# Kernel tuning notes

Hardware: AMD Instinct MI355X
Metric: run time of the kernel (lower is better)

The kernel has to match this reference:

```python
import jax, jax.numpy as jnp
import numpy as np

H, P, T = 256, 16, 4      # hidden_size, maxout_pool_size, max_dec_steps
B, M = 32, 600            # batch, document length

def _lstm_cell(x, h, c, W_ih, W_hh, b_ih, b_hh):
    g = x @ W_ih.T + b_ih + h @ W_hh.T + b_hh
    i, f, gg, o = jnp.split(g, 4, axis=1)  # torch gate order i,f,g,o
    c = jax.nn.sigmoid(f) * c + jax.nn.sigmoid(i) * jnp.tanh(gg)
    h = jax.nn.sigmoid(o) * jnp.tanh(c)
    return h, c

def _maxout(h, U, u_cat, mask_mult, W_lin, W1, b1, W2, b2, W12, b12):
    b, m, _ = U.shape
    r = jnp.tanh(jnp.concatenate([h, u_cat], axis=1) @ W_lin.T)                  # [b,H]
    m1_in = jnp.concatenate([U, jnp.broadcast_to(r[:, None, :], (b, m, H))], 2)  # [b,m,3H]
    m1 = (m1_in @ W1.T + b1).reshape(b, m, H, P).max(-1)                         # [b,m,H]
    m2 = (m1 @ W2.T + b2).reshape(b, m, H, P).max(-1)                            # [b,m,H]
    alpha = (jnp.concatenate([m1, m2], axis=2) @ W12.T + b12).max(-1)            # [b,m]
    return jax.nn.log_softmax(alpha + mask_mult, axis=1)

def _forward(U, d_mask, span, W_ih, W_hh, b_ih, b_hh,
             Ws_lin, Ws_m1, bs_m1, Ws_m2, bs_m2, Ws_m12, bs_m12,
             We_lin, We_m1, be_m1, We_m2, be_m2, We_m12, be_m12):
    b, m, _ = U.shape
    idxb = jnp.arange(b)
    mask_mult = (1.0 - d_mask.astype(U.dtype)) * -1e30
    s_i = jnp.zeros(b, jnp.int32)
    e_i = (jnp.sum(d_mask, 1) - 1).astype(jnp.int32)
    s_tgt, e_tgt = span[:, 0], span[:, 1]
    h = jnp.zeros((b, H), U.dtype)
    c = jnp.zeros((b, H), U.dtype)
    mask_s = mask_e = None
    res_s, res_e, res_ms, res_me, losses = [], [], [], [], []
    u_s = U[idxb, s_i]
    for t in range(T):
        u_e = U[idxb, e_i]
        u_cat = jnp.concatenate([u_s, u_e], axis=1)
        h, c = _lstm_cell(u_cat, h, c, W_ih, W_hh, b_ih, b_hh)
        # start pointer
        lsm = _maxout(h, U, u_cat, mask_mult, Ws_lin, Ws_m1, bs_m1, Ws_m2, bs_m2, Ws_m12, bs_m12)
        idx = jnp.argmax(lsm, axis=1).astype(jnp.int32)
        if t == 0:
            mask_s = jnp.ones(b, bool)
        else:
            idx = idx * mask_s.astype(jnp.int32)
            prev = s_i * mask_s.astype(jnp.int32)
            mask_s = idx != prev
        loss_s = jnp.mean(-jnp.take_along_axis(lsm, s_tgt[:, None], 1)[:, 0]) * mask_s.astype(U.dtype)
        s_i = idx
        u_s = U[idxb, s_i]
        # end pointer
        u_cat2 = jnp.concatenate([u_s, u_e], axis=1)
        lsm_e = _maxout(h, U, u_cat2, mask_mult, We_lin, We_m1, be_m1, We_m2, be_m2, We_m12, be_m12)
        idx_e = jnp.argmax(lsm_e, axis=1).astype(jnp.int32)
        if t == 0:
            mask_e = jnp.ones(b, bool)
        else:
            idx_e = idx_e * mask_e.astype(jnp.int32)
            prev_e = e_i * mask_e.astype(jnp.int32)
            mask_e = idx_e != prev_e
        loss_e = jnp.mean(-jnp.take_along_axis(lsm_e, e_tgt[:, None], 1)[:, 0]) * mask_e.astype(U.dtype)
        e_i = idx_e
        losses.append(loss_s + loss_e)
        res_s.append(s_i); res_ms.append(mask_s)
        res_e.append(e_i); res_me.append(mask_e)
    pos_s = jnp.sum(jnp.stack(res_ms, 1).astype(jnp.int32), 1) - 1
    p1 = jnp.take_along_axis(jnp.stack(res_s, 1), pos_s[:, None], 1)[:, 0]
    pos_e = jnp.sum(jnp.stack(res_me, 1).astype(jnp.int32), 1) - 1
    p2 = jnp.take_along_axis(jnp.stack(res_e, 1), pos_e[:, None], 1)[:, 0]
    loss = jnp.mean(jnp.sum(jnp.stack(losses, 1), 1) / T)
    return loss, p1, p2

def setup_inputs():
    key = jax.random.key(0)
    ks = jax.random.split(key, 16)
    U = jax.random.normal(ks[0], (B, M, 2 * H), jnp.float32)
    lengths = jax.random.randint(ks[1], (B,), M // 2, M + 1)
    d_mask = (jnp.arange(M)[None, :] < lengths[:, None]).astype(jnp.int32)
    span = jax.random.randint(ks[2], (B, 2), 0, M // 2).astype(jnp.int32)
    def w(k, shape, fan_in):
        return (jax.random.normal(k, shape, jnp.float32) / np.float32(np.sqrt(fan_in)))
    b_ih = jnp.zeros(4 * H, jnp.float32).at[H:2 * H].set(1.0)  # forget-gate bias init
    params = {
        'W_ih': w(ks[3], (4 * H, 4 * H), 4 * H), 'W_hh': w(ks[4], (4 * H, H), H),
        'b_ih': b_ih, 'b_hh': jnp.zeros(4 * H, jnp.float32),
        'Ws_lin': w(ks[5], (H, 5 * H), 5 * H),
        'Ws_m1': w(ks[6], (H * P, 3 * H), 3 * H), 'bs_m1': jnp.zeros(H * P, jnp.float32),
        'Ws_m2': w(ks[7], (H * P, H), H), 'bs_m2': jnp.zeros(H * P, jnp.float32),
        'Ws_m12': w(ks[8], (P, 2 * H), 2 * H), 'bs_m12': jnp.zeros(P, jnp.float32),
        'We_lin': w(ks[9], (H, 5 * H), 5 * H),
        'We_m1': w(ks[10], (H * P, 3 * H), 3 * H), 'be_m1': jnp.zeros(H * P, jnp.float32),
        'We_m2': w(ks[11], (H * P, H), H), 'be_m2': jnp.zeros(H * P, jnp.float32),
        'We_m12': w(ks[12], (P, 2 * H), 2 * H), 'be_m12': jnp.zeros(P, jnp.float32),
    }
    return {'U': U, 'd_mask': d_mask, 'span': span, **params}

def reference(U, d_mask, span, W_ih, W_hh, b_ih, b_hh,
              Ws_lin, Ws_m1, bs_m1, Ws_m2, bs_m2, Ws_m12, bs_m12,
              We_lin, We_m1, be_m1, We_m2, be_m2, We_m12, be_m12):
    return _forward(U, d_mask, span, W_ih, W_hh, b_ih, b_hh,
                    Ws_lin, Ws_m1, bs_m1, Ws_m2, bs_m2, Ws_m12, bs_m12,
                    We_lin, We_m1, be_m1, We_m2, be_m2, We_m12, be_m12)
```

## Files before the change

### kernel.cpp

```cpp
#include <hip/hip_runtime.h>
#include <math.h>

namespace {

typedef unsigned short u16;
typedef __attribute__((ext_vector_type(4))) float f32x4;
typedef __attribute__((ext_vector_type(8))) _Float16 f16x8;
typedef __attribute__((ext_vector_type(4))) _Float16 f16x4;
typedef __attribute__((ext_vector_type(2))) _Float16 f16x2;

constexpr int B = 32;
constexpr int M = 600;
constexpr int H = 256;
constexpr int TSTEPS = 4;
constexpr int HP = 4096;
constexpr int BM = B * M;
constexpr int TWOH = 512;
constexpr int THREEH = 768;
constexpr int FOURH = 1024;
constexpr int FIVEH = 1280;
constexpr int NTILES = BM / 128;

__device__ __forceinline__ float sigf(float x) { return 1.0f / (1.0f + expf(-x)); }

__device__ __forceinline__ void gload16(const u16* g, u16* l) {
    __builtin_amdgcn_global_load_lds(
        (const __attribute__((address_space(1))) void*)g,
        (__attribute__((address_space(3))) void*)l, 16, 0, 0);
}

__global__ void k_init(const int* __restrict__ d_mask,
                       float* __restrict__ h, float* __restrict__ c,
                       float* __restrict__ loss_vec,
                       int* __restrict__ s_i, int* __restrict__ e_i,
                       int* __restrict__ p1r, int* __restrict__ p2r)
{
    int tid = threadIdx.x;
    for (int i = tid; i < B * H; i += 256) { h[i] = 0.f; c[i] = 0.f; }
    if (tid < B) {
        loss_vec[tid] = 0.f;
        s_i[tid] = 0;
        int s = 0;
        const int* row = d_mask + tid * M;
        for (int m = 0; m < M; ++m) s += row[m];
        e_i[tid] = s - 1;
        p1r[tid] = 0; p2r[tid] = 0;
    }
}

__global__ __launch_bounds__(128) void k_flags(const int* __restrict__ d_mask,
                                               int* __restrict__ flags)
{
    int bm = blockIdx.x * 128 + threadIdx.x;
    int cnt = __syncthreads_count(d_mask[bm]);
    if (threadIdx.x == 0) flags[blockIdx.x] = (cnt == 0) ? 1 : 0;
}

__global__ __launch_bounds__(256) void k_gather(
    const float* __restrict__ U, const int* __restrict__ s_i,
    const int* __restrict__ e_i, float* __restrict__ u_cat)
{
    int idx = blockIdx.x * 256 + threadIdx.x;
    int b = idx >> 9, k = idx & 511;
    u_cat[b * FOURH + k]       = U[((size_t)b * M + s_i[b]) * TWOH + k];
    u_cat[b * FOURH + 512 + k] = U[((size_t)b * M + e_i[b]) * TWOH + k];
}

__global__ __launch_bounds__(256) void k_lstm_gemm2(
    const float* __restrict__ U, const int* __restrict__ s_i,
    const int* __restrict__ e_i, const float* __restrict__ h,
    const float* __restrict__ W_ih, const float* __restrict__ W_hh,
    const float* __restrict__ b_ih, const float* __restrict__ b_hh,
    float* __restrict__ g)
{
    int idx = blockIdx.x * 256 + threadIdx.x;
    int b = idx >> 10, j = idx & 1023;
    const float* us = U + ((size_t)b * M + s_i[b]) * TWOH;
    const float* ue = U + ((size_t)b * M + e_i[b]) * TWOH;
    float acc = 0.f;
    const float4* x4 = (const float4*)us;
    const float4* wi4 = (const float4*)(W_ih + (size_t)j * FOURH);
    #pragma unroll 4
    for (int k = 0; k < TWOH / 4; ++k) {
        float4 a = x4[k], w = wi4[k];
        acc += a.x * w.x + a.y * w.y + a.z * w.z + a.w * w.w;
    }
    const float4* y4 = (const float4*)ue;
    const float4* wi4b = wi4 + TWOH / 4;
    #pragma unroll 4
    for (int k = 0; k < TWOH / 4; ++k) {
        float4 a = y4[k], w = wi4b[k];
        acc += a.x * w.x + a.y * w.y + a.z * w.z + a.w * w.w;
    }
    const float4* h4 = (const float4*)(h + b * H);
    const float4* wh4 = (const float4*)(W_hh + (size_t)j * H);
    #pragma unroll 4
    for (int k = 0; k < H / 4; ++k) {
        float4 a = h4[k], w = wh4[k];
        acc += a.x * w.x + a.y * w.y + a.z * w.z + a.w * w.w;
    }
    g[idx] = acc + b_ih[j] + b_hh[j];
}

__global__ __launch_bounds__(256) void k_lstm_gemm(
    const float* __restrict__ u_cat, const float* __restrict__ h,
    const float* __restrict__ W_ih, const float* __restrict__ W_hh,
    const float* __restrict__ b_ih, const float* __restrict__ b_hh,
    float* __restrict__ g)
{
    int idx = blockIdx.x * 256 + threadIdx.x;
    int b = idx >> 10, j = idx & 1023;
    float acc = 0.f;
    const float4* x4 = (const float4*)(u_cat + b * FOURH);
    const float4* wi4 = (const float4*)(W_ih + (size_t)j * FOURH);
    #pragma unroll 4
    for (int k = 0; k < FOURH / 4; ++k) {
        float4 a = x4[k], w = wi4[k];
        acc += a.x * w.x + a.y * w.y + a.z * w.z + a.w * w.w;
    }
    const float4* h4 = (const float4*)(h + b * H);
    const float4* wh4 = (const float4*)(W_hh + (size_t)j * H);
    #pragma unroll 4
    for (int k = 0; k < H / 4; ++k) {
        float4 a = h4[k], w = wh4[k];
        acc += a.x * w.x + a.y * w.y + a.z * w.z + a.w * w.w;
    }
    g[idx] = acc + b_ih[j] + b_hh[j];
}

__global__ __launch_bounds__(256) void k_lstm_gates(
    const float* __restrict__ g, float* __restrict__ h, float* __restrict__ c)
{
    int idx = blockIdx.x * 256 + threadIdx.x;
    int b = idx >> 8, i = idx & (H - 1);
    const float* gr = g + b * FOURH;
    float gi = gr[i], gf = gr[H + i], gg = gr[2 * H + i], go = gr[3 * H + i];
    float cn = sigf(gf) * c[idx] + sigf(gi) * tanhf(gg);
    c[idx] = cn;
    h[idx] = sigf(go) * tanhf(cn);
}

__global__ __launch_bounds__(256) void k_r2(
    const float* __restrict__ h, const float* __restrict__ U,
    const int* __restrict__ s_i, const int* __restrict__ e_i,
    const float* __restrict__ W_lin, float* __restrict__ r)
{
    int gid = blockIdx.x * 256 + threadIdx.x;
    int out = gid >> 2;
    int part = gid & 3;
    int b = out >> 8, i = out & (H - 1);
    const float4* w4 = (const float4*)(W_lin + (size_t)i * FIVEH);
    const float4* h4 = (const float4*)(h + b * H);
    const float4* us4 = (const float4*)(U + ((size_t)b * M + s_i[b]) * TWOH);
    const float4* ue4 = (const float4*)(U + ((size_t)b * M + e_i[b]) * TWOH);
    float acc = 0.f;
    int k0 = part * 80;
    #pragma unroll 4
    for (int kk = k0; kk < k0 + 80; ++kk) {
        float4 a;
        if (kk < 64) a = h4[kk];
        else if (kk < 192) a = us4[kk - 64];
        else a = ue4[kk - 192];
        float4 ww = w4[kk];
        acc += a.x * ww.x + a.y * ww.y + a.z * ww.z + a.w * ww.w;
    }
    acc += __shfl_xor(acc, 1);
    acc += __shfl_xor(acc, 2);
    if (part == 0) r[out] = tanhf(acc);
}

__global__ __launch_bounds__(256) void k_r(
    const float* __restrict__ h, const float* __restrict__ u_cat,
    const float* __restrict__ W_lin, float* __restrict__ r)
{
    int idx = blockIdx.x * 256 + threadIdx.x;
    int b = idx >> 8, i = idx & (H - 1);
    const float* w = W_lin + (size_t)i * FIVEH;
    float acc = 0.f;
    const float4* h4 = (const float4*)(h + b * H);
    const float4* w4 = (const float4*)w;
    #pragma unroll 4
    for (int k = 0; k < H / 4; ++k) {
        float4 a = h4[k], ww = w4[k];
        acc += a.x * ww.x + a.y * ww.y + a.z * ww.z + a.w * ww.w;
    }
    const float4* x4 = (const float4*)(u_cat + b * FOURH);
    const float4* w4b = (const float4*)(w + H);
    #pragma unroll 4
    for (int k = 0; k < FOURH / 4; ++k) {
        float4 a = x4[k], ww = w4b[k];
        acc += a.x * ww.x + a.y * ww.y + a.z * ww.z + a.w * ww.w;
    }
    r[idx] = tanhf(acc);
}

__global__ __launch_bounds__(256) void k_rW(
    const float* __restrict__ r, const float* __restrict__ W1,
    const float* __restrict__ b1, float* __restrict__ rW)
{
    int idx = blockIdx.x * 256 + threadIdx.x;
    int b = idx >> 12, j = idx & (HP - 1);
    const float4* r4 = (const float4*)(r + b * H);
    const float4* w4 = (const float4*)(W1 + (size_t)j * THREEH + TWOH);
    float acc = 0.f;
    #pragma unroll 4
    for (int k = 0; k < H / 4; ++k) {
        float4 a = r4[k], w = w4[k];
        acc += a.x * w.x + a.y * w.y + a.z * w.z + a.w * w.w;
    }
    rW[idx] = acc + b1[j];
}

__global__ __launch_bounds__(256) void k_rW2h(
    const float* __restrict__ r, const _Float16* __restrict__ Wt,
    const float* __restrict__ b1, float* __restrict__ rW)
{
    const int b = blockIdx.y;
    const int j = (blockIdx.x * 256 + threadIdx.x) * 2;
    __shared__ float sr[256];
    sr[threadIdx.x] = r[b * H + threadIdx.x];
    __syncthreads();
    float a0 = b1[j], a1 = b1[j + 1];
    #pragma unroll 4
    for (int k = 0; k < H; ++k) {
        f16x2 wv = *(const f16x2*)(Wt + (size_t)k * HP + j);
        float x = sr[k];
        a0 += x * (float)wv[0];
        a1 += x * (float)wv[1];
    }
    rW[(size_t)b * HP + j]     = a0;
    rW[(size_t)b * HP + j + 1] = a1;
}

__global__ __launch_bounds__(256) void k_transp2(
    const float* __restrict__ W, _Float16* __restrict__ Wt)
{
    __shared__ float s[32][33];
    int j0 = (blockIdx.x & 127) << 5;
    int k0 = (blockIdx.x >> 7) << 5;
    int tx = threadIdx.x & 31, ty = threadIdx.x >> 5;
    #pragma unroll
    for (int kk = 0; kk < 4; ++kk) {
        int jl = ty + kk * 8;
        s[jl][tx] = W[(size_t)(j0 + jl) * THREEH + TWOH + k0 + tx];
    }
    __syncthreads();
    #pragma unroll
    for (int kk = 0; kk < 4; ++kk) {
        int kl = ty + kk * 8;
        Wt[(size_t)(k0 + kl) * HP + j0 + tx] = (_Float16)s[tx][kl];
    }
}

__global__ __launch_bounds__(256) void k_cvtH(
    const float* __restrict__ src, int ld, int Kc, _Float16* __restrict__ dst)
{
    int i4 = blockIdx.x * 256 + threadIdx.x;
    int perrow = Kc >> 2;
    int row = i4 / perrow;
    int kc = (i4 - row * perrow) << 2;
    float4 v = *(const float4*)(src + (size_t)row * ld + kc);
    f16x4 o;
    o[0] = (_Float16)v.x; o[1] = (_Float16)v.y; o[2] = (_Float16)v.z; o[3] = (_Float16)v.w;
    *(f16x4*)(dst + (size_t)row * Kc + kc) = o;
}

template <int EPI>
__global__ __launch_bounds__(256, 4) void gemmJ(
    const _Float16* __restrict__ A, const _Float16* __restrict__ Bw,
    int K, const float* __restrict__ extra, const int* __restrict__ skip,
    float* __restrict__ Cf, _Float16* __restrict__ Ch)
{
    const int nwgx = gridDim.x;
    const int nwg  = nwgx * gridDim.y;
    int bid = blockIdx.y * nwgx + blockIdx.x;
    const int cpx = nwg >> 3;
    bid = (bid & 7) * cpx + (bid >> 3);
    const int bx = bid % nwgx, by = bid / nwgx;

    if (skip[by]) return;
    __shared__ __align__(16) u16 sA[2][128 * 32];
    __shared__ __align__(16) u16 sB[2][128 * 32];
    const int tid = threadIdx.x;
    const int w = tid >> 6, lane = tid & 63;
    const int row0 = by * 128, col0 = bx * 128;
    const int wm = w & 1, wn = w >> 1;

    const int r1g = tid >> 2,        k1 = (tid & 3) ^ ((r1g >> 1) & 3);
    const int r2g = (tid + 256) >> 2, k2 = ((tid + 256) & 3) ^ ((r2g >> 1) & 3);
    const size_t gA1 = (size_t)(row0 + r1g) * K + k1 * 8;
    const size_t gA2 = (size_t)(row0 + r2g) * K + k2 * 8;
    const size_t gB1 = (size_t)(col0 + r1g) * K + k1 * 8;
    const size_t gB2 = (size_t)(col0 + r2g) * K + k2 * 8;

    f32x4 acc[4][4] = {};

    gload16((const u16*)(A  + gA1), &sA[0][tid * 8]);
    gload16((const u16*)(A  + gA2), &sA[0][(tid + 256) * 8]);
    gload16((const u16*)(Bw + gB1), &sB[0][tid * 8]);
    gload16((const u16*)(Bw + gB2), &sB[0][(tid + 256) * 8]);

    const int iters = K >> 5;
    const int mrow = lane & 15;
    const int kg = lane >> 4;
    const int slot = kg ^ ((mrow >> 1) & 3);
    const int eoff = slot << 3;

    for (int it = 0; it < iters; ++it) {
        const int cur = it & 1;
        __syncthreads();
        if (it + 1 < iters) {
            const int k0n = (it + 1) << 5;
            gload16((const u16*)(A  + gA1 + k0n), &sA[1 - cur][tid * 8]);
            gload16((const u16*)(A  + gA2 + k0n), &sA[1 - cur][(tid + 256) * 8]);
            gload16((const u16*)(Bw + gB1 + k0n), &sB[1 - cur][tid * 8]);
            gload16((const u16*)(Bw + gB2 + k0n), &sB[1 - cur][(tid + 256) * 8]);
        }
        const u16* pa = &sA[cur][(wm * 64 + mrow) * 32 + eoff];
        const u16* pb = &sB[cur][(wn * 64 + mrow) * 32 + eoff];
        f16x8 fa[4], fb[4];
        #pragma unroll
        for (int f = 0; f < 4; ++f) {
            fa[f] = *(const f16x8*)(pa + f * 16 * 32);
            fb[f] = *(const f16x8*)(pb + f * 16 * 32);
        }
        #pragma unroll
        for (int i = 0; i < 4; ++i) {
            #pragma unroll
            for (int j = 0; j < 4; ++j) {
                acc[i][j] = __builtin_amdgcn_mfma_f32_16x16x32_f16(fa[i], fb[j], acc[i][j], 0, 0, 0);
            }
        }
    }

    const int cq = lane & 15, rq = lane >> 4;
    if (EPI == 4) {
        #pragma unroll
        for (int i = 0; i < 4; ++i) {
            #pragma unroll
            for (int j = 0; j < 4; ++j) {
                int col = col0 + wn * 64 + j * 16 + cq;
                #pragma unroll
                for (int rr = 0; rr < 4; ++rr) {
                    int row = row0 + wm * 64 + i * 16 + rq * 4 + rr;
                    Ch[(size_t)row * HP + col] = (_Float16)acc[i][j][rr];
                }
            }
        }
    } else if (EPI == 1) {
        #pragma unroll
        for (int j = 0; j < 4; ++j) {
            int col = col0 + wn * 64 + j * 16 + cq;
            int gcol = (col0 >> 4) + wn * 4 + j;
            float bv = extra[col];
            #pragma unroll
            for (int i = 0; i < 4; ++i) {
                #pragma unroll
                for (int rr = 0; rr < 4; ++rr) {
                    float v = acc[i][j][rr] + bv;
                    v = fmaxf(v, __shfl_xor(v, 1));
                    v = fmaxf(v, __shfl_xor(v, 2));
                    v = fmaxf(v, __shfl_xor(v, 4));
                    v = fmaxf(v, __shfl_xor(v, 8));
                    if (cq == 0) {
                        int row = row0 + wm * 64 + i * 16 + rq * 4 + rr;
                        Ch[(size_t)row * H + gcol] = (_Float16)v;
                    }
                }
            }
        }
    } else {
        const int rbase = row0 + wm * 64;
        const int b0 = rbase / M;
        const int bnd = (b0 + 1) * M;
        #pragma unroll
        for (int j = 0; j < 4; ++j) {
            int col = col0 + wn * 64 + j * 16 + cq;
            int gcol = (col0 >> 4) + wn * 4 + j;
            float e0 = extra[(size_t)b0 * HP + col];
            float e1 = extra[(size_t)(b0 + 1) * HP + col];
            #pragma unroll
            for (int i = 0; i < 4; ++i) {
                #pragma unroll
                for (int rr = 0; rr < 4; ++rr) {
                    int row = rbase + i * 16 + rq * 4 + rr;
                    float v = acc[i][j][rr] + ((row >= bnd) ? e1 : e0);
                    v = fmaxf(v, __shfl_xor(v, 1));
                    v = fmaxf(v, __shfl_xor(v, 2));
                    v = fmaxf(v, __shfl_xor(v, 4));
                    v = fmaxf(v, __shfl_xor(v, 8));
                    if (cq == 0)
                        Ch[(size_t)row * H + gcol] = (_Float16)v;
                }
            }
        }
    }
}

__global__ __launch_bounds__(256) void k_m1A16(
    const _Float16* __restrict__ A, const float* __restrict__ rW,
    _Float16* __restrict__ m1)
{
    int idx = blockIdx.x * 256 + threadIdx.x;
    int bm = idx >> 8;
    int h = idx & (H - 1);
    int b = bm / M;
    const f16x8* a8 = (const f16x8*)(A + (size_t)bm * HP + (h << 4));
    const float4* r4 = (const float4*)(rW + (size_t)b * HP + (h << 4));
    f16x8 a0 = a8[0], a1 = a8[1];
    float4 ra = r4[0], rb = r4[1], rc = r4[2], rd = r4[3];
    float mx;
    mx = fmaxf(fmaxf(fmaxf((float)a0[0] + ra.x, (float)a0[1] + ra.y),
                     fmaxf((float)a0[2] + ra.z, (float)a0[3] + ra.w)),
         fmaxf(fmaxf((float)a0[4] + rb.x, (float)a0[5] + rb.y),
               fmaxf((float)a0[6] + rb.z, (float)a0[7] + rb.w)));
    mx = fmaxf(mx,
         fmaxf(fmaxf(fmaxf((float)a1[0] + rc.x, (float)a1[1] + rc.y),
                     fmaxf((float)a1[2] + rc.z, (float)a1[3] + rc.w)),
               fmaxf(fmaxf((float)a1[4] + rd.x, (float)a1[5] + rd.y),
                     fmaxf((float)a1[6] + rd.z, (float)a1[7] + rd.w))));
    m1[idx] = (_Float16)mx;
}

template <int EPI>
__global__ __launch_bounds__(256) void gemm64(
    const float* __restrict__ Ag, int lda,
    const float* __restrict__ Bg, int ldb,
    const float* __restrict__ extra,
    float* __restrict__ C, int K, int ldc)
{
    __shared__ float As[16][68];
    __shared__ float Bs[16][68];
    const int tid = threadIdx.x;
    const int tx = tid & 15;
    const int ty = tid >> 4;
    const int row0 = blockIdx.y * 64;
    const int col0 = blockIdx.x * 64;
    const int lr = tid >> 2;
    const int lk = (tid & 3) << 2;
    const float* Aload = Ag + (size_t)(row0 + lr) * lda + lk;
    const float* Bload = Bg + (size_t)(col0 + lr) * ldb + lk;
    float acc[4][4] = {};
    for (int k0 = 0; k0 < K; k0 += 16) {
        float4 av = *(const float4*)(Aload + k0);
        float4 bv = *(const float4*)(Bload + k0);
        __syncthreads();
        As[lk + 0][lr] = av.x; As[lk + 1][lr] = av.y; As[lk + 2][lr] = av.z; As[lk + 3][lr] = av.w;
        Bs[lk + 0][lr] = bv.x; Bs[lk + 1][lr] = bv.y; Bs[lk + 2][lr] = bv.z; Bs[lk + 3][lr] = bv.w;
        __syncthreads();
        #pragma unroll
        for (int k = 0; k < 16; ++k) {
            float4 a4 = *(const float4*)(&As[k][ty << 2]);
            float4 b4 = *(const float4*)(&Bs[k][tx << 2]);
            acc[0][0] += a4.x * b4.x; acc[0][1] += a4.x * b4.y; acc[0][2] += a4.x * b4.z; acc[0][3] += a4.x * b4.w;
            acc[1][0] += a4.y * b4.x; acc[1][1] += a4.y * b4.y; acc[1][2] += a4.y * b4.z; acc[1][3] += a4.y * b4.w;
            acc[2][0] += a4.z * b4.x; acc[2][1] += a4.z * b4.y; acc[2][2] += a4.z * b4.z; acc[2][3] += a4.z * b4.w;
            acc[3][0] += a4.w * b4.x; acc[3][1] += a4.w * b4.y; acc[3][2] += a4.w * b4.z; acc[3][3] += a4.w * b4.w;
        }
    }
    if (EPI == 1) {
        const int cb = col0 + (tx << 2);
        float b0 = extra[cb], b1v = extra[cb + 1], b2v = extra[cb + 2], b3v = extra[cb + 3];
        #pragma unroll
        for (int i = 0; i < 4; ++i) {
            float mth = fmaxf(fmaxf(acc[i][0] + b0, acc[i][1] + b1v),
                              fmaxf(acc[i][2] + b2v, acc[i][3] + b3v));
            float r1 = fmaxf(mth, __shfl_xor(mth, 1));
            float r2 = fmaxf(r1, __shfl_xor(r1, 2));
            if ((tx & 3) == 0)
                C[(size_t)(row0 + (ty << 2) + i) * ldc + (col0 >> 4) + (tx >> 2)] = r2;
        }
    } else if (EPI == 2) {
        const int cb = col0 + (tx << 2);
        #pragma unroll
        for (int i = 0; i < 4; ++i) {
            int row = row0 + (ty << 2) + i;
            int b = row / M;
            const float* rw = extra + (size_t)b * HP + cb;
            float mth = fmaxf(fmaxf(acc[i][0] + rw[0], acc[i][1] + rw[1]),
                              fmaxf(acc[i][2] + rw[2], acc[i][3] + rw[3]));
            float r1 = fmaxf(mth, __shfl_xor(mth, 1));
            float r2 = fmaxf(r1, __shfl_xor(r1, 2));
            if ((tx & 3) == 0)
                C[(size_t)row * ldc + (col0 >> 4) + (tx >> 2)] = r2;
        }
    }
}

__global__ __launch_bounds__(256) void k_alpha(
    const float* __restrict__ m1, const float* __restrict__ m2,
    const float* __restrict__ W12, const float* __restrict__ b12,
    const int* __restrict__ d_mask, float* __restrict__ alpha)
{
    __shared__ float Ws[16 * 512];
    const int tid = threadIdx.x;
    for (int i = tid; i < 16 * 512; i += 256) Ws[i] = W12[i];
    __syncthreads();
    const int wave = tid >> 6, lane = tid & 63;
    const int bm = blockIdx.x * 4 + wave;
    const float* r1 = m1 + (size_t)bm * H;
    const float* r2 = m2 + (size_t)bm * H;
    float acc[16] = {};
    #pragma unroll
    for (int q = 0; q < 4; ++q) {
        int k = lane + (q << 6);
        float x = r1[k];
        #pragma unroll
        for (int p = 0; p < 16; ++p) acc[p] += x * Ws[p * 512 + k];
    }
    #pragma unroll
    for (int q = 0; q < 4; ++q) {
        int k = lane + (q << 6);
        float x = r2[k];
        #pragma unroll
        for (int p = 0; p < 16; ++p) acc[p] += x * Ws[p * 512 + 256 + k];
    }
    #pragma unroll
    for (int p = 0; p < 16; ++p) {
        float v = acc[p];
        v += __shfl_xor(v, 1);  v += __shfl_xor(v, 2);  v += __shfl_xor(v, 4);
        v += __shfl_xor(v, 8);  v += __shfl_xor(v, 16); v += __shfl_xor(v, 32);
        acc[p] = v;
    }
    if (lane == 0) {
        float mx = -INFINITY;
        #pragma unroll
        for (int p = 0; p < 16; ++p) mx = fmaxf(mx, acc[p] + b12[p]);
        alpha[bm] = d_mask[bm] ? mx : -1e30f;
    }
}

__global__ __launch_bounds__(256) void k_alphaM(
    const _Float16* __restrict__ m1, const _Float16* __restrict__ m2,
    const _Float16* __restrict__ W12h, const float* __restrict__ b12,
    const int* __restrict__ d_mask, float* __restrict__ alpha)
{
    const int wave = threadIdx.x >> 6, lane = threadIdx.x & 63;
    const int bm0 = blockIdx.x * 64 + wave * 16;
    const int rsel = lane & 15, kg = lane >> 4;
    f16x8 fb[16];
    #pragma unroll
    for (int kb = 0; kb < 16; ++kb)
        fb[kb] = *(const f16x8*)(W12h + (size_t)rsel * 512 + kb * 32 + kg * 8);
    f32x4 acc = {};
    const _Float16* r1 = m1 + (size_t)(bm0 + rsel) * H + kg * 8;
    const _Float16* r2 = m2 + (size_t)(bm0 + rsel) * H + kg * 8;
    #pragma unroll
    for (int kb = 0; kb < 8; ++kb) {
        f16x8 fa = *(const f16x8*)(r1 + kb * 32);
        acc = __builtin_amdgcn_mfma_f32_16x16x32_f16(fa, fb[kb], acc, 0, 0, 0);
    }
    #pragma unroll
    for (int kb = 0; kb < 8; ++kb) {
        f16x8 fa = *(const f16x8*)(r2 + kb * 32);
        acc = __builtin_amdgcn_mfma_f32_16x16x32_f16(fa, fb[8 + kb], acc, 0, 0, 0);
    }
    const int cq = lane & 15, rq = lane >> 4;
    float bv = b12[cq];
    #pragma unroll
    for (int reg = 0; reg < 4; ++reg) {
        float v = acc[reg] + bv;
        v = fmaxf(v, __shfl_xor(v, 1));
        v = fmaxf(v, __shfl_xor(v, 2));
        v = fmaxf(v, __shfl_xor(v, 4));
        v = fmaxf(v, __shfl_xor(v, 8));
        if (cq == 0) {
            int bm = bm0 + rq * 4 + reg;
            alpha[bm] = d_mask[bm] ? v : -1e30f;
        }
    }
}

__global__ __launch_bounds__(1024) void k_smu(
    const float* __restrict__ alpha, const int* __restrict__ span, int phase,
    int* __restrict__ pos, int* __restrict__ mask,
    int* __restrict__ prun, float* __restrict__ loss_vec, int t)
{
    __shared__ float s_loss[B];
    __shared__ int s_idx[B];
    const int wave = threadIdx.x >> 6, lane = threadIdx.x & 63;
    for (int b = wave; b < B; b += 16) {
        const float* row = alpha + b * M;
        float best = -INFINITY; int bidx = 0;
        for (int m = lane; m < M; m += 64) {
            float v = row[m];
            if (v > best) { best = v; bidx = m; }
        }
        #pragma unroll
        for (int off = 1; off < 64; off <<= 1) {
            float v2 = __shfl_xor(best, off);
            int i2 = __shfl_xor(bidx, off);
            if (v2 > best || (v2 == best && i2 < bidx)) { best = v2; bidx = i2; }
        }
        float ps = 0.f;
        for (int m = lane; m < M; m += 64) ps += expf(row[m] - best);
        #pragma unroll
        for (int off = 32; off > 0; off >>= 1) ps += __shfl_xor(ps, off);
        if (lane == 0) {
            float lse = best + logf(ps);
            int tgt = span[b * 2 + phase];
            s_loss[b] = -(row[tgt] - lse);
            s_idx[b] = bidx;
        }
    }
    __syncthreads();
    if (wave == 0) {
        int b = lane;
        int active = (b < B) ? 1 : 0;
        int ni = 0, nm = 0;
        if (active) {
            int id = s_idx[b];
            if (t == 0) { nm = 1; ni = id; }
            else {
                int om = mask[b];
                ni = id * om;
                int prev = pos[b] * om;
                nm = (ni != prev) ? 1 : 0;
            }
        }
        float v = active ? s_loss[b] : 0.f;
        #pragma unroll
        for (int off = 32; off > 0; off >>= 1) v += __shfl_xor(v, off);
        float S = v * (1.0f / (float)B);
        if (active) {
            pos[b] = ni;
            mask[b] = nm;
            if (nm) { prun[b] = ni; loss_vec[b] += S; }
        }
    }
}

__global__ __launch_bounds__(256) void k_softmax(
    const float* __restrict__ alpha, const int* __restrict__ span, int phase,
    float* __restrict__ loss_term, int* __restrict__ idx_out)
{
    __shared__ float sv[256];
    __shared__ int si[256];
    const int b = blockIdx.x, tid = threadIdx.x;
    const float* row = alpha + b * M;
    float best = -INFINITY; int bidx = 0;
    for (int m = tid; m < M; m += 256) {
        float v = row[m];
        if (v > best) { best = v; bidx = m; }
    }
    sv[tid] = best; si[tid] = bidx;
    __syncthreads();
    for (int s = 128; s > 0; s >>= 1) {
        if (tid < s) {
            float v2 = sv[tid + s]; int i2 = si[tid + s];
            if (v2 > sv[tid] || (v2 == sv[tid] && i2 < si[tid])) { sv[tid] = v2; si[tid] = i2; }
        }
        __syncthreads();
    }
    float bmax = sv[0]; int amax = si[0];
    __syncthreads();
    float ps = 0.f;
    for (int m = tid; m < M; m += 256) ps += expf(row[m] - bmax);
    sv[tid] = ps;
    __syncthreads();
    for (int s = 128; s > 0; s >>= 1) {
        if (tid < s) sv[tid] += sv[tid + s];
        __syncthreads();
    }
    if (tid == 0) {
        float lse = bmax + logf(sv[0]);
        int tgt = span[b * 2 + phase];
        loss_term[b] = -(row[tgt] - lse);
        idx_out[b] = amax;
    }
}

__global__ void k_update(const int* __restrict__ idx_in, const float* __restrict__ loss_term,
                         int* __restrict__ pos, int* __restrict__ mask,
                         int* __restrict__ prun, float* __restrict__ loss_vec, int t)
{
    int b = threadIdx.x;
    int active = (b < B) ? 1 : 0;
    int ni = 0, nm = 0;
    if (active) {
        int id = idx_in[b];
        if (t == 0) { nm = 1; ni = id; }
        else {
            int om = mask[b];
            ni = id * om;
            int prev = pos[b] * om;
            nm = (ni != prev) ? 1 : 0;
        }
    }
    float v = active ? loss_term[b] : 0.f;
    #pragma unroll
    for (int off = 32; off > 0; off >>= 1) v += __shfl_xor(v, off);
    float S = v * (1.0f / (float)B);
    if (active) {
        pos[b] = ni;
        mask[b] = nm;
        if (nm) { prun[b] = ni; loss_vec[b] += S; }
    }
}

__global__ void k_finalize(const float* __restrict__ loss_vec, const int* __restrict__ p1r,
                           const int* __restrict__ p2r, float* __restrict__ out)
{
    int b = threadIdx.x;
    float v = (b < B) ? loss_vec[b] : 0.f;
    #pragma unroll
    for (int off = 32; off > 0; off >>= 1) v += __shfl_xor(v, off);
    if (b == 0) out[0] = v / (float)(B * TSTEPS);
    if (b < B) {
        out[1 + b] = (float)p1r[b];
        out[1 + B + b] = (float)p2r[b];
    }
}

}

extern "C" void kernel_launch(void* const* d_in, const int* in_sizes, int n_in,
                              void* d_out, int out_size, void* d_ws, size_t ws_size,
                              hipStream_t stream)
{
    const float* U      = (const float*)d_in[0];
    const int*   d_mask = (const int*)d_in[1];
    const int*   span   = (const int*)d_in[2];
    const float* W_ih   = (const float*)d_in[3];
    const float* W_hh   = (const float*)d_in[4];
    const float* b_ih   = (const float*)d_in[5];
    const float* b_hh   = (const float*)d_in[6];
    const float* Ws_lin = (const float*)d_in[7];
    const float* Ws_m1  = (const float*)d_in[8];
    const float* bs_m1  = (const float*)d_in[9];
    const float* Ws_m2  = (const float*)d_in[10];
    const float* bs_m2  = (const float*)d_in[11];
    const float* Ws_m12 = (const float*)d_in[12];
    const float* bs_m12 = (const float*)d_in[13];
    const float* We_lin = (const float*)d_in[14];
    const float* We_m1  = (const float*)d_in[15];
    const float* be_m1  = (const float*)d_in[16];
    const float* We_m2  = (const float*)d_in[17];
    const float* be_m2  = (const float*)d_in[18];
    const float* We_m12 = (const float*)d_in[19];
    const float* be_m12 = (const float*)d_in[20];

    float* ws = (float*)d_ws;
    size_t o = 0;
    float* m2b   = ws + o; o += (size_t)BM * H;
    float* alphab= ws + o; o += BM;
    float* u_cat = ws + o; o += B * FOURH;
    float* gbuf  = ws + o; o += B * FOURH;
    float* hbuf  = ws + o; o += B * H;
    float* cbuf  = ws + o; o += B * H;
    float* rbuf  = ws + o; o += B * H;
    float* rWb   = ws + o; o += B * HP;
    float* loss_term = ws + o; o += B;
    float* loss_vec  = ws + o; o += B;
    int* ib = (int*)(ws + o); o += 8 * B + 160;
    int* idxb   = ib + 0 * B;
    int* s_i    = ib + 1 * B;
    int* e_i    = ib + 2 * B;
    int* mask_s = ib + 3 * B;
    int* mask_e = ib + 4 * B;
    int* p1r    = ib + 5 * B;
    int* p2r    = ib + 6 * B;
    int* flags  = ib + 8 * B;
    size_t o_common = (o + 3) & ~(size_t)3;

    float* m1b = ws + o_common;

    _Float16* hs = (_Float16*)(ws + o_common);
    size_t q = 0;
    _Float16* Uh    = hs + q; q += (size_t)BM * TWOH;
    _Float16* W1s   = hs + q; q += (size_t)HP * TWOH;
    _Float16* W1e   = hs + q; q += (size_t)HP * TWOH;
    _Float16* W2s   = hs + q; q += (size_t)HP * H;
    _Float16* W2e   = hs + q; q += (size_t)HP * H;
    _Float16* m1b16 = hs + q; q += (size_t)BM * H;
    _Float16* Wth_s = hs + q; q += (size_t)H * HP;
    _Float16* Wth_e = hs + q; q += (size_t)H * HP;
    _Float16* W12sh = hs + q; q += 16 * 512;
    _Float16* W12eh = hs + q; q += 16 * 512;
    q = (q + 7) & ~(size_t)7;
    const size_t need2 = o_common * sizeof(float) + q * sizeof(_Float16);
    _Float16* A_s16 = hs + q;
    _Float16* A_e16 = A_s16 + (size_t)BM * HP;
    const size_t need15s = need2 + (size_t)BM * HP * sizeof(_Float16);
    const size_t need16  = need15s + (size_t)BM * HP * sizeof(_Float16);

    _Float16* m2h = (_Float16*)m2b;

    const int tier = (ws_size >= need16) ? 16
                   : (ws_size >= need15s) ? 15
                   : (ws_size >= need2) ? 2 : 3;

    k_init<<<1, 256, 0, stream>>>(d_mask, hbuf, cbuf, loss_vec, s_i, e_i, p1r, p2r);

    if (tier != 3) {
        k_flags<<<NTILES, 128, 0, stream>>>(d_mask, flags);
        k_cvtH<<<BM * TWOH / 4 / 256, 256, 0, stream>>>(U, TWOH, TWOH, Uh);
        k_cvtH<<<HP * TWOH / 4 / 256, 256, 0, stream>>>(Ws_m1, THREEH, TWOH, W1s);
        k_cvtH<<<HP * TWOH / 4 / 256, 256, 0, stream>>>(We_m1, THREEH, TWOH, W1e);
        k_cvtH<<<HP * H / 4 / 256, 256, 0, stream>>>(Ws_m2, H, H, W2s);
        k_cvtH<<<HP * H / 4 / 256, 256, 0, stream>>>(We_m2, H, H, W2e);
        k_cvtH<<<16 * 512 / 4 / 256, 256, 0, stream>>>(Ws_m12, 512, 512, W12sh);
        k_cvtH<<<16 * 512 / 4 / 256, 256, 0, stream>>>(We_m12, 512, 512, W12eh);
        k_transp2<<<1024, 256, 0, stream>>>(Ws_m1, Wth_s);
        k_transp2<<<1024, 256, 0, stream>>>(We_m1, Wth_e);

        dim3 gJ(HP / 128, NTILES);
        if (tier >= 15) {
            gemmJ<4><<<gJ, 256, 0, stream>>>(Uh, W1s, TWOH, nullptr, flags, nullptr, A_s16);
        }
        if (tier == 16) {
            gemmJ<4><<<gJ, 256, 0, stream>>>(Uh, W1e, TWOH, nullptr, flags, nullptr, A_e16);
        }

        for (int t = 0; t < TSTEPS; ++t) {
            k_lstm_gemm2<<<128, 256, 0, stream>>>(U, s_i, e_i, hbuf, W_ih, W_hh, b_ih, b_hh, gbuf);
            k_lstm_gates<<<32, 256, 0, stream>>>(gbuf, hbuf, cbuf);

            k_r2<<<128, 256, 0, stream>>>(hbuf, U, s_i, e_i, Ws_lin, rbuf);
            k_rW2h<<<dim3(HP / 512, B), 256, 0, stream>>>(rbuf, Wth_s, bs_m1, rWb);
            if (tier >= 15)
                k_m1A16<<<BM * H / 256, 256, 0, stream>>>(A_s16, rWb, m1b16);
            else
                gemmJ<3><<<gJ, 256, 0, stream>>>(Uh, W1s, TWOH, rWb, flags, nullptr, m1b16);
            gemmJ<1><<<gJ, 256, 0, stream>>>(m1b16, W2s, H, bs_m2, flags, nullptr, m2h);
            k_alphaM<<<BM / 64, 256, 0, stream>>>(m1b16, m2h, W12sh, bs_m12, d_mask, alphab);
            k_smu<<<1, 1024, 0, stream>>>(alphab, span, 0, s_i, mask_s, p1r, loss_vec, t);

            k_r2<<<128, 256, 0, stream>>>(hbuf, U, s_i, e_i, We_lin, rbuf);
            k_rW2h<<<dim3(HP / 512, B), 256, 0, stream>>>(rbuf, Wth_e, be_m1, rWb);
            if (tier == 16)
                k_m1A16<<<BM * H / 256, 256, 0, stream>>>(A_e16, rWb, m1b16);
            else
                gemmJ<3><<<gJ, 256, 0, stream>>>(Uh, W1e, TWOH, rWb, flags, nullptr, m1b16);
            gemmJ<1><<<gJ, 256, 0, stream>>>(m1b16, W2e, H, be_m2, flags, nullptr, m2h);
            k_alphaM<<<BM / 64, 256, 0, stream>>>(m1b16, m2h, W12eh, be_m12, d_mask, alphab);
            k_smu<<<1, 1024, 0, stream>>>(alphab, span, 1, e_i, mask_e, p2r, loss_vec, t);
        }
    } else {
        dim3 gemm_grid(HP / 64, BM / 64);
        for (int t = 0; t < TSTEPS; ++t) {
            k_gather<<<64, 256, 0, stream>>>(U, s_i, e_i, u_cat);
            k_lstm_gemm<<<128, 256, 0, stream>>>(u_cat, hbuf, W_ih, W_hh, b_ih, b_hh, gbuf);
            k_lstm_gates<<<32, 256, 0, stream>>>(gbuf, hbuf, cbuf);

            k_r<<<32, 256, 0, stream>>>(hbuf, u_cat, Ws_lin, rbuf);
            k_rW<<<512, 256, 0, stream>>>(rbuf, Ws_m1, bs_m1, rWb);
            gemm64<2><<<gemm_grid, 256, 0, stream>>>(U, TWOH, Ws_m1, THREEH, rWb, m1b, TWOH, H);
            gemm64<1><<<gemm_grid, 256, 0, stream>>>(m1b, H, Ws_m2, H, bs_m2, m2b, H, H);
            k_alpha<<<BM / 4, 256, 0, stream>>>(m1b, m2b, Ws_m12, bs_m12, d_mask, alphab);
            k_softmax<<<B, 256, 0, stream>>>(alphab, span, 0, loss_term, idxb);
            k_update<<<1, 64, 0, stream>>>(idxb, loss_term, s_i, mask_s, p1r, loss_vec, t);

            k_gather<<<64, 256, 0, stream>>>(U, s_i, e_i, u_cat);

            k_r<<<32, 256, 0, stream>>>(hbuf, u_cat, We_lin, rbuf);
            k_rW<<<512, 256, 0, stream>>>(rbuf, We_m1, be_m1, rWb);
            gemm64<2><<<gemm_grid, 256, 0, stream>>>(U, TWOH, We_m1, THREEH, rWb, m1b, TWOH, H);
            gemm64<1><<<gemm_grid, 256, 0, stream>>>(m1b, H, We_m2, H, be_m2, m2b, H, H);
            k_alpha<<<BM / 4, 256, 0, stream>>>(m1b, m2b, We_m12, be_m12, d_mask, alphab);
            k_softmax<<<B, 256, 0, stream>>>(alphab, span, 1, loss_term, idxb);
            k_update<<<1, 64, 0, stream>>>(idxb, loss_term, e_i, mask_e, p2r, loss_vec, t);
        }
    }

    k_finalize<<<1, 64, 0, stream>>>(loss_vec, p1r, p2r, (float*)d_out);
}
```

Before: 2.416 ms.

## Triple-buffer LDS in gemmJ with partial vmcnt waits for deeper prefetch

New measurement: 2.544 ms. 1.05x slower.

```diff
diff --git a/kernel.cpp b/kernel.cpp
--- a/kernel.cpp
+++ b/kernel.cpp
@@ -279,8 +279,8 @@
     const int bx = bid % nwgx, by = bid / nwgx;
 
     if (skip[by]) return;
-    __shared__ __align__(16) u16 sA[2][128 * 32];
-    __shared__ __align__(16) u16 sB[2][128 * 32];
+    __shared__ __align__(16) u16 sA[3][128 * 32];
+    __shared__ __align__(16) u16 sB[3][128 * 32];
     const int tid = threadIdx.x;
     const int w = tid >> 6, lane = tid & 63;
     const int row0 = by * 128, col0 = bx * 128;
@@ -294,28 +294,30 @@
     const size_t gB2 = (size_t)(col0 + r2g) * K + k2 * 8;
 
     f32x4 acc[4][4] = {};
-
-    gload16((const u16*)(A  + gA1), &sA[0][tid * 8]);
-    gload16((const u16*)(A  + gA2), &sA[0][(tid + 256) * 8]);
-    gload16((const u16*)(Bw + gB1), &sB[0][tid * 8]);
-    gload16((const u16*)(Bw + gB2), &sB[0][(tid + 256) * 8]);
-
     const int iters = K >> 5;
+
+    auto stage = [&](int itx, int bufi) {
+        const int k0n = itx << 5;
+        gload16((const u16*)(A  + gA1 + k0n), &sA[bufi][tid * 8]);
+        gload16((const u16*)(A  + gA2 + k0n), &sA[bufi][(tid + 256) * 8]);
+        gload16((const u16*)(Bw + gB1 + k0n), &sB[bufi][tid * 8]);
+        gload16((const u16*)(Bw + gB2 + k0n), &sB[bufi][(tid + 256) * 8]);
+    };
+    stage(0, 0);
+    if (iters > 1) stage(1, 1);
+
     const int mrow = lane & 15;
     const int kg = lane >> 4;
     const int slot = kg ^ ((mrow >> 1) & 3);
     const int eoff = slot << 3;
 
+    int cur = 0, pre = 2;
     for (int it = 0; it < iters; ++it) {
-        const int cur = it & 1;
-        __syncthreads();
-        if (it + 1 < iters) {
-            const int k0n = (it + 1) << 5;
-            gload16((const u16*)(A  + gA1 + k0n), &sA[1 - cur][tid * 8]);
-            gload16((const u16*)(A  + gA2 + k0n), &sA[1 - cur][(tid + 256) * 8]);
-            gload16((const u16*)(Bw + gB1 + k0n), &sB[1 - cur][tid * 8]);
-            gload16((const u16*)(Bw + gB2 + k0n), &sB[1 - cur][(tid + 256) * 8]);
-        }
+        if (it + 1 < iters)
+            asm volatile("s_waitcnt vmcnt(4)\n\ts_barrier" ::: "memory");
+        else
+            asm volatile("s_waitcnt vmcnt(0)\n\ts_barrier" ::: "memory");
+        if (it + 2 < iters) stage(it + 2, pre);
         const u16* pa = &sA[cur][(wm * 64 + mrow) * 32 + eoff];
         const u16* pb = &sB[cur][(wn * 64 + mrow) * 32 + eoff];
         f16x8 fa[4], fb[4];
@@ -331,6 +333,8 @@
                 acc[i][j] = __builtin_amdgcn_mfma_f32_16x16x32_f16(fa[i], fb[j], acc[i][j], 0, 0, 0);
             }
         }
+        cur = (cur == 2) ? 0 : cur + 1;
+        pre = (pre == 2) ? 0 : pre + 1;
     }
 
     const int cq = lane & 15, rq = lane >> 4;
```
